# Kernel tuning notes

Hardware: AMD Instinct MI355X
Metric: run time of the kernel (lower is better)

The kernel has to match this reference:

```python
import jax, jax.numpy as jnp
import numpy as np

N = 100000
E = 1600000
D_IN = 128
D_HID = 128
D_OUT = 64


def setup_inputs() -> dict:
    key = jax.random.key(0)
    ks = jax.random.split(key, 9)
    x = jax.random.normal(ks[0], (N, D_IN), dtype=jnp.float32)
    edge_index = jax.random.randint(ks[1], (2, E), 0, N, dtype=jnp.int64)
    edge_weight = jax.random.uniform(ks[2], (E,), dtype=jnp.float32)
    s1 = 1.0 / np.sqrt(D_IN)
    s2 = 1.0 / np.sqrt(D_HID)
    W1 = jax.random.uniform(ks[3], (D_IN, D_HID), jnp.float32, -s1, s1)
    b1 = jnp.zeros((D_HID,), jnp.float32)
    W2 = jax.random.uniform(ks[4], (D_HID, D_HID), jnp.float32, -s2, s2)
    b2 = jnp.zeros((D_HID,), jnp.float32)
    Wfc = jax.random.uniform(ks[5], (D_HID, D_OUT), jnp.float32, -s2, s2)
    bfc = jax.random.uniform(ks[6], (D_OUT,), jnp.float32, -s2, s2)
    return {"x": x, "edge_index": edge_index, "edge_weight": edge_weight,
            "W1": W1, "b1": b1, "W2": W2, "b2": b2, "Wfc": Wfc, "bfc": bfc}


def _gcn_layer(h, row, col, w, n, W, b):
    # h' = D^{-1/2} (A + I) D^{-1/2} h W + b  (PyG GCNConv with edge weights)
    h = h @ W  # [n, d_out]
    deg = jax.ops.segment_sum(w, col, num_segments=n)  # weighted in-degree incl. self loops
    dinv = jnp.where(deg > 0, jax.lax.rsqrt(deg), 0.0)
    norm = dinv[row] * w * dinv[col]  # [E+n]
    out = jax.ops.segment_sum(norm[:, None] * h[row], col, num_segments=n)
    return out + b


def reference(x, edge_index, edge_weight, W1, b1, W2, b2, Wfc, bfc):
    n = x.shape[0]
    loop = jnp.arange(n, dtype=edge_index.dtype)
    row = jnp.concatenate([edge_index[0], loop])  # sources (+ self loops)
    col = jnp.concatenate([edge_index[1], loop])  # destinations
    w = jnp.concatenate([edge_weight, jnp.ones((n,), edge_weight.dtype)])
    h = jax.nn.relu(_gcn_layer(x, row, col, w, n, W1, b1))
    h = jax.nn.relu(_gcn_layer(h, row, col, w, n, W2, b2))
    return jax.nn.sigmoid(h @ Wfc + bfc)
```

## Files before the change

### kernel.cpp

```cpp
#include <hip/hip_runtime.h>
#include <math.h>

#define N_NODES 100000
#define N_EDGES 1600000
#define SCAN_CHUNK 1024
#define NSCAN ((N_NODES + SCAN_CHUNK - 1) / SCAN_CHUNK)
#define WMASK ((1ull << 40) - 1)
#define LDSW 136

typedef short bf16x8 __attribute__((ext_vector_type(8)));
typedef float f32x4 __attribute__((ext_vector_type(4)));

__device__ __forceinline__ float2 bf2f(unsigned int u) {
    float2 r;
    r.x = __uint_as_float(u << 16);
    r.y = __uint_as_float(u & 0xffff0000u);
    return r;
}
__device__ __forceinline__ unsigned int f2bf2(float a, float b) {
    unsigned int ua = __float_as_uint(a), ub = __float_as_uint(b);
    ua += 0x7fffu + ((ua >> 16) & 1u);
    ub += 0x7fffu + ((ub >> 16) & 1u);
    return (ua >> 16) | (ub & 0xffff0000u);
}
__device__ __forceinline__ unsigned short f2bf(float a) {
    unsigned int u = __float_as_uint(a);
    u += 0x7fffu + ((u >> 16) & 1u);
    return (unsigned short)(u >> 16);
}

__global__ void k_detect(const int* __restrict__ ei, int* __restrict__ flag, int host_hint) {
    __shared__ int s_cnt;
    if (threadIdx.x == 0) s_cnt = 0;
    __syncthreads();
    int local = 0;
    for (int e = threadIdx.x; e < 4096; e += blockDim.x)
        if (ei[2 * e + 1] != 0) local++;
    atomicAdd(&s_cnt, local);
    __syncthreads();
    if (threadIdx.x == 0) flag[0] = (host_hint || s_cnt < 100) ? 1 : 0;
}

__global__ void k_init(unsigned long long* __restrict__ packed) {
    int i = blockIdx.x * blockDim.x + threadIdx.x;
    if (i < N_NODES) packed[i] = 0ull;
}

__global__ void k_hist(const int* __restrict__ ei32, const int* __restrict__ flag,
                       const float* __restrict__ w,
                       unsigned long long* __restrict__ packed) {
    int e = blockIdx.x * blockDim.x + threadIdx.x;
    if (e >= N_EDGES) return;
    int c;
    if (flag[0]) {
        const long long* ei64 = (const long long*)ei32;
        c = (int)ei64[N_EDGES + e];
    } else {
        c = ei32[N_EDGES + e];
    }
    unsigned long long wfix = (unsigned long long)(w[e] * 4294967296.0f);
    atomicAdd(&packed[c], (1ull << 40) | wfix);
}

__global__ __launch_bounds__(256) void k_scan_a(const unsigned long long* __restrict__ packed,
                                                int* __restrict__ cnt,
                                                float* __restrict__ dinv,
                                                int* __restrict__ bsum) {
    __shared__ int sred[4];
    const int b = blockIdx.x, tid = threadIdx.x;
    const int base = b * SCAN_CHUNK;
    int s = 0;
    #pragma unroll
    for (int i = 0; i < 4; i++) {
        int idx = base + tid + i * 256;
        if (idx < N_NODES) {
            unsigned long long p = packed[idx];
            int c = (int)(p >> 40);
            float deg = 1.0f + (float)(p & WMASK) * 2.3283064365386963e-10f;
            cnt[idx] = c;
            dinv[idx] = rsqrtf(deg);
            s += c;
        }
    }
    #pragma unroll
    for (int sh = 1; sh < 64; sh <<= 1) s += __shfl_xor(s, sh);
    if ((tid & 63) == 0) sred[tid >> 6] = s;
    __syncthreads();
    if (tid == 0) bsum[b] = sred[0] + sred[1] + sred[2] + sred[3];
}

__global__ __launch_bounds__(128) void k_scan_b(const int* __restrict__ bsum,
                                                int* __restrict__ bex) {
    __shared__ int wsum[2];
    const int tid = threadIdx.x, lane = tid & 63, w = tid >> 6;
    int v = (tid < NSCAN) ? bsum[tid] : 0;
    int x = v;
    #pragma unroll
    for (int sh = 1; sh < 64; sh <<= 1) {
        int t = __shfl_up(x, sh);
        if (lane >= sh) x += t;
    }
    if (lane == 63) wsum[w] = x;
    __syncthreads();
    int add = (w == 1) ? wsum[0] : 0;
    if (tid < NSCAN) bex[tid] = x - v + add;
}

__global__ __launch_bounds__(256) void k_scan_c(const int* __restrict__ cnt,
                                                const int* __restrict__ bex,
                                                int* __restrict__ off,
                                                int* __restrict__ cur) {
    __shared__ int swave[4];
    const int b = blockIdx.x, tid = threadIdx.x;
    const int base = b * SCAN_CHUNK + tid * 4;
    int4 v = make_int4(0, 0, 0, 0);
    if (base + 3 < N_NODES) v = *(const int4*)&cnt[base];
    else {
        if (base + 0 < N_NODES) v.x = cnt[base + 0];
        if (base + 1 < N_NODES) v.y = cnt[base + 1];
        if (base + 2 < N_NODES) v.z = cnt[base + 2];
    }
    const int tsum = v.x + v.y + v.z + v.w;
    const int lane = tid & 63, w = tid >> 6;
    int x = tsum;
    #pragma unroll
    for (int sh = 1; sh < 64; sh <<= 1) {
        int t = __shfl_up(x, sh);
        if (lane >= sh) x += t;
    }
    if (lane == 63) swave[w] = x;
    __syncthreads();
    int wadd = 0;
    for (int i = 0; i < w; i++) wadd += swave[i];
    const int ex = bex[b] + wadd + (x - tsum);
    const int p0 = ex, p1 = p0 + v.x, p2 = p1 + v.y, p3 = p2 + v.z;
    if (base + 3 < N_NODES) {
        *(int4*)&off[base] = make_int4(p0, p1, p2, p3);
        *(int4*)&cur[base] = make_int4(p0, p1, p2, p3);
    } else {
        if (base + 0 < N_NODES) { off[base + 0] = p0; cur[base + 0] = p0; }
        if (base + 1 < N_NODES) { off[base + 1] = p1; cur[base + 1] = p1; }
        if (base + 2 < N_NODES) { off[base + 2] = p2; cur[base + 2] = p2; }
    }
}

__global__ void k_scatter(const int* __restrict__ ei32, const int* __restrict__ flag,
                          const float* __restrict__ w, const float* __restrict__ dinv,
                          int* __restrict__ cursor, unsigned int* __restrict__ sedge) {
    int e = blockIdx.x * blockDim.x + threadIdx.x;
    if (e >= N_EDGES) return;
    int r, c;
    if (flag[0]) {
        const long long* ei64 = (const long long*)ei32;
        r = (int)ei64[e];
        c = (int)ei64[N_EDGES + e];
    } else {
        r = ei32[e];
        c = ei32[N_EDGES + e];
    }
    float coef = dinv[r] * w[e] * dinv[c];
    unsigned int q = (unsigned int)(coef * 32767.0f + 0.5f);
    int p = atomicAdd(&cursor[c], 1);
    sedge[p] = ((unsigned int)r << 15) | q;
}

__global__ void k_castw(const float* __restrict__ W, unsigned short* __restrict__ Wt) {
    int i = blockIdx.x * blockDim.x + threadIdx.x;
    int k = i >> 7, n = i & 127;
    Wt[n * 128 + k] = f2bf(W[k * 128 + n]);
}

template <bool ABF16>
__global__ __launch_bounds__(256) void k_gemm_mfma(const void* __restrict__ Av,
                                                   const unsigned short* __restrict__ Wt,
                                                   unsigned short* __restrict__ Cb) {
    __shared__ unsigned short Al[128 * LDSW];
    __shared__ unsigned short Wl[128 * LDSW];
    const int tid = threadIdx.x;
    const int srow = tid >> 1, h = tid & 1;
    const int r0 = blockIdx.x * 128;

    {
        const uint4* src = (const uint4*)&Wt[srow * 128 + h * 64];
        uint4* dst = (uint4*)&Wl[srow * LDSW + h * 64];
        #pragma unroll
        for (int c = 0; c < 8; c++) dst[c] = src[c];
    }
    {
        const bool ok = (r0 + srow) < N_NODES;
        uint4* dst = (uint4*)&Al[srow * LDSW + h * 64];
        if constexpr (ABF16) {
            const uint4* src = (const uint4*)((const unsigned short*)Av +
                                              (size_t)(r0 + srow) * 128 + h * 64);
            uint4 z = make_uint4(0, 0, 0, 0);
            #pragma unroll
            for (int c = 0; c < 8; c++) dst[c] = ok ? src[c] : z;
        } else {
            const float* src = (const float*)Av + (size_t)(r0 + srow) * 128 + h * 64;
            #pragma unroll
            for (int c = 0; c < 8; c++) {
                float4 f0 = ok ? *(const float4*)&src[c * 8]     : make_float4(0, 0, 0, 0);
                float4 f1 = ok ? *(const float4*)&src[c * 8 + 4] : make_float4(0, 0, 0, 0);
                uint4 pk;
                pk.x = f2bf2(f0.x, f0.y);
                pk.y = f2bf2(f0.z, f0.w);
                pk.z = f2bf2(f1.x, f1.y);
                pk.w = f2bf2(f1.z, f1.w);
                dst[c] = pk;
            }
        }
    }
    __syncthreads();

    const int lane = tid & 63;
    const int w = tid >> 6;
    const int lr = lane & 15;
    const int kg = lane >> 4;
    f32x4 acc[2][8] = {};

    #pragma unroll
    for (int k0 = 0; k0 < 128; k0 += 32) {
        const int kb = k0 + kg * 8;
        bf16x8 a0 = *(const bf16x8*)&Al[(w * 32 + lr) * LDSW + kb];
        bf16x8 a1 = *(const bf16x8*)&Al[(w * 32 + 16 + lr) * LDSW + kb];
        #pragma unroll
        for (int ct = 0; ct < 8; ct++) {
            bf16x8 b = *(const bf16x8*)&Wl[(ct * 16 + lr) * LDSW + kb];
            acc[0][ct] = __builtin_amdgcn_mfma_f32_16x16x32_bf16(a0, b, acc[0][ct], 0, 0, 0);
            acc[1][ct] = __builtin_amdgcn_mfma_f32_16x16x32_bf16(a1, b, acc[1][ct], 0, 0, 0);
        }
    }

    #pragma unroll
    for (int rt = 0; rt < 2; rt++)
        #pragma unroll
        for (int r = 0; r < 4; r++) {
            int row = r0 + w * 32 + rt * 16 + kg * 4 + r;
            if (row < N_NODES) {
                #pragma unroll
                for (int ct = 0; ct < 8; ct++)
                    Cb[(size_t)row * 128 + ct * 16 + lr] = f2bf(acc[rt][ct][r]);
            }
        }
}

template <int DOUT>
__global__ __launch_bounds__(256) void k_gemm(const float* __restrict__ A,
                                              const float* __restrict__ W,
                                              const float* __restrict__ bias,
                                              float* __restrict__ C) {
    constexpr int CPT = DOUT / 16;
    __shared__ float Ws[128 * DOUT];
    __shared__ float As[8][128];
    const int tid = threadIdx.x;
    const int tx = tid & 15, ty = tid >> 4;

    for (int i = tid * 4; i < 128 * DOUT; i += 256 * 4)
        *(float4*)&Ws[i] = *(const float4*)&W[i];

    const int r0 = blockIdx.x * 128;
    const int arow = tid >> 1;
    const int ak = (tid & 1) * 4;
    const bool rowok = (r0 + arow) < N_NODES;

    float acc[8][CPT];
    #pragma unroll
    for (int i = 0; i < 8; i++)
        #pragma unroll
        for (int j = 0; j < CPT; j++) acc[i][j] = 0.f;

    for (int k0 = 0; k0 < 128; k0 += 8) {
        float4 av = make_float4(0.f, 0.f, 0.f, 0.f);
        if (rowok) av = *(const float4*)&A[(size_t)(r0 + arow) * 128 + k0 + ak];
        __syncthreads();
        As[ak + 0][arow] = av.x;
        As[ak + 1][arow] = av.y;
        As[ak + 2][arow] = av.z;
        As[ak + 3][arow] = av.w;
        __syncthreads();
        #pragma unroll
        for (int kk = 0; kk < 8; kk++) {
            float4 a0 = *(const float4*)&As[kk][ty * 8];
            float4 a1 = *(const float4*)&As[kk][ty * 8 + 4];
            float av8[8] = {a0.x, a0.y, a0.z, a0.w, a1.x, a1.y, a1.z, a1.w};
            float wv[CPT];
            float4 w0 = *(const float4*)&Ws[(k0 + kk) * DOUT + tx * CPT];
            wv[0] = w0.x; wv[1] = w0.y; wv[2] = w0.z; wv[3] = w0.w;
            #pragma unroll
            for (int i = 0; i < 8; i++)
                #pragma unroll
                for (int j = 0; j < CPT; j++)
                    acc[i][j] = fmaf(av8[i], wv[j], acc[i][j]);
        }
    }

    #pragma unroll
    for (int i = 0; i < 8; i++) {
        int r = r0 + ty * 8 + i;
        if (r < N_NODES) {
            float vout[CPT];
            #pragma unroll
            for (int j = 0; j < CPT; j++) {
                float v = acc[i][j] + bias[tx * CPT + j];
                vout[j] = 1.0f / (1.0f + expf(-v));
            }
            #pragma unroll
            for (int j = 0; j < CPT; j += 4)
                *(float4*)&C[(size_t)r * DOUT + tx * CPT + j] =
                    make_float4(vout[j], vout[j + 1], vout[j + 2], vout[j + 3]);
        }
    }
}

template <bool OBF16>
__global__ __launch_bounds__(256) void k_aggregate(const unsigned int* __restrict__ lin,
                                                   const unsigned int* __restrict__ sedge,
                                                   const int* __restrict__ off,
                                                   const int* __restrict__ cnt,
                                                   const float* __restrict__ dinv,
                                                   const float* __restrict__ bias,
                                                   void* __restrict__ outv) {
    const int node = (blockIdx.x * 256 + threadIdx.x) >> 6;
    const int lane = threadIdx.x & 63;
    if (node >= N_NODES) return;
    const float di = dinv[node];
    float2 sv = bf2f(lin[(size_t)node * 64 + lane]);
    float ax = di * di * sv.x;
    float ay = di * di * sv.y;
    const int start = __builtin_amdgcn_readfirstlane(off[node]);
    const int end = start + __builtin_amdgcn_readfirstlane(cnt[node]);
    for (int e0 = start; e0 < end; e0 += 8) {
        unsigned int en[8];
        #pragma unroll
        for (int i = 0; i < 8; i++) {
            int idx = e0 + i;
            en[i] = sedge[idx < end ? idx : end - 1];
        }
        float2 v[8];
        #pragma unroll
        for (int i = 0; i < 8; i++)
            v[i] = bf2f(lin[(size_t)(en[i] >> 15) * 64 + lane]);
        #pragma unroll
        for (int i = 0; i < 8; i++) {
            float cf = (e0 + i < end) ? (float)(en[i] & 0x7fffu) * 3.051850947599719e-05f : 0.0f;
            ax = fmaf(cf, v[i].x, ax);
            ay = fmaf(cf, v[i].y, ay);
        }
    }
    const int lane2 = lane * 2;
    float2 bv = *(const float2*)&bias[lane2];
    ax = fmaxf(ax + bv.x, 0.f);
    ay = fmaxf(ay + bv.y, 0.f);
    if constexpr (OBF16) {
        ((unsigned int*)outv)[(size_t)node * 64 + lane] = f2bf2(ax, ay);
    } else {
        *(float2*)&((float*)outv)[(size_t)node * 128 + lane2] = make_float2(ax, ay);
    }
}

extern "C" void kernel_launch(void* const* d_in, const int* in_sizes, int n_in,
                              void* d_out, int out_size, void* d_ws, size_t ws_size,
                              hipStream_t stream) {
    const float* x   = (const float*)d_in[0];
    const int*   ei  = (const int*)d_in[1];
    const float* ew  = (const float*)d_in[2];
    const float* W1  = (const float*)d_in[3];
    const float* b1  = (const float*)d_in[4];
    const float* W2  = (const float*)d_in[5];
    const float* b2  = (const float*)d_in[6];
    const float* Wfc = (const float*)d_in[7];
    const float* bfc = (const float*)d_in[8];
    float* out = (float*)d_out;

    char* ws = (char*)d_ws;
    size_t o = 0;
    auto alloc = [&](size_t bytes) { char* p = ws + o; o += (bytes + 255) & ~255ull; return p; };
    unsigned long long* packed = (unsigned long long*)alloc((size_t)N_NODES * 8);
    float* dinv  = (float*)alloc((size_t)N_NODES * 4);
    int*   cnt   = (int*)  alloc((size_t)N_NODES * 4);
    int*   off   = (int*)  alloc((size_t)N_NODES * 4);
    int*   cur   = (int*)  alloc((size_t)N_NODES * 4);
    int*   flag  = (int*)  alloc(256);
    int*   bsum  = (int*)  alloc((size_t)NSCAN * 4);
    int*   bex   = (int*)  alloc((size_t)NSCAN * 4);
    unsigned int*   sedge = (unsigned int*)alloc((size_t)N_EDGES * 4);
    unsigned short* W1t   = (unsigned short*)alloc(128 * 128 * 2);
    unsigned short* W2t   = (unsigned short*)alloc(128 * 128 * 2);
    unsigned short* hbf   = (unsigned short*)alloc((size_t)N_NODES * 128 * 2);
    unsigned short* aggb  = (unsigned short*)alloc((size_t)N_NODES * 128 * 2);
    float*          aggf  = (float*)alloc((size_t)N_NODES * 128 * 4);

    const int EB = (N_EDGES + 255) / 256;
    const int NB = (N_NODES + 255) / 256;

    int hint64 = (in_sizes[1] == 4 * N_EDGES) ? 1 : 0;
    k_detect<<<1, 256, 0, stream>>>(ei, flag, hint64);
    k_init<<<NB, 256, 0, stream>>>(packed);
    k_castw<<<64, 256, 0, stream>>>(W1, W1t);
    k_castw<<<64, 256, 0, stream>>>(W2, W2t);
    k_hist<<<EB, 256, 0, stream>>>(ei, flag, ew, packed);
    k_scan_a<<<NSCAN, 256, 0, stream>>>(packed, cnt, dinv, bsum);
    k_scan_b<<<1, 128, 0, stream>>>(bsum, bex);
    k_scan_c<<<NSCAN, 256, 0, stream>>>(cnt, bex, off, cur);
    k_scatter<<<EB, 256, 0, stream>>>(ei, flag, ew, dinv, cur, sedge);

    const int GB = (N_NODES + 127) / 128;
    const int AB = (N_NODES * 64 + 255) / 256;

    k_gemm_mfma<false><<<GB, 256, 0, stream>>>(x, W1t, hbf);
    k_aggregate<true><<<AB, 256, 0, stream>>>((const unsigned int*)hbf, sedge, off, cnt, dinv, b1, aggb);
    k_gemm_mfma<true><<<GB, 256, 0, stream>>>(aggb, W2t, hbf);
    k_aggregate<false><<<AB, 256, 0, stream>>>((const unsigned int*)hbf, sedge, off, cnt, dinv, b2, aggf);
    k_gemm<64><<<GB, 256, 0, stream>>>(aggf, Wfc, bfc, out);
}
```

Before: 480.7 us.

## Bin edges by destination range before CSR scatter to localize writes

```diff
diff --git a/kernel.cpp b/kernel.cpp
--- a/kernel.cpp
+++ b/kernel.cpp
@@ -7,6 +7,11 @@
 #define NSCAN ((N_NODES + SCAN_CHUNK - 1) / SCAN_CHUNK)
 #define WMASK ((1ull << 40) - 1)
 #define LDSW 136
+#define BINSHIFT 9
+#define NBINS 196
+#define BINCAP 12288
+#define BIN_BLOCKS 512
+#define EPT 13
 
 typedef short bf16x8 __attribute__((ext_vector_type(8)));
 typedef float f32x4 __attribute__((ext_vector_type(4)));
@@ -41,25 +46,65 @@
     if (threadIdx.x == 0) flag[0] = (host_hint || s_cnt < 100) ? 1 : 0;
 }
 
-__global__ void k_init(unsigned long long* __restrict__ packed) {
+__global__ void k_init(unsigned long long* __restrict__ packed, int* __restrict__ gbincur) {
     int i = blockIdx.x * blockDim.x + threadIdx.x;
     if (i < N_NODES) packed[i] = 0ull;
-}
-
-__global__ void k_hist(const int* __restrict__ ei32, const int* __restrict__ flag,
-                       const float* __restrict__ w,
-                       unsigned long long* __restrict__ packed) {
-    int e = blockIdx.x * blockDim.x + threadIdx.x;
-    if (e >= N_EDGES) return;
-    int c;
-    if (flag[0]) {
-        const long long* ei64 = (const long long*)ei32;
-        c = (int)ei64[N_EDGES + e];
-    } else {
-        c = ei32[N_EDGES + e];
-    }
-    unsigned long long wfix = (unsigned long long)(w[e] * 4294967296.0f);
-    atomicAdd(&packed[c], (1ull << 40) | wfix);
+    if (i < NBINS) gbincur[i] = i * BINCAP;
+}
+
+__global__ __launch_bounds__(256) void k_bin(const int* __restrict__ ei32,
+                                             const int* __restrict__ flag,
+                                             const float* __restrict__ ew,
+                                             unsigned long long* __restrict__ packed,
+                                             int* __restrict__ gbincur,
+                                             uint2* __restrict__ binstage) {
+    __shared__ int scnt[256];
+    __shared__ int sbase[256];
+    const int tid = threadIdx.x;
+    scnt[tid] = 0;
+    const bool f64 = flag[0] != 0;
+    const long long base = (long long)blockIdx.x * (256 * EPT);
+    unsigned int ea[EPT], eb[EPT];
+    __syncthreads();
+    #pragma unroll
+    for (int i = 0; i < EPT; i++) {
+        long long e = base + (long long)i * 256 + tid;
+        bool ok = e < N_EDGES;
+        int r = 0, c = 0;
+        float w = 0.f;
+        if (ok) {
+            if (f64) {
+                const long long* p64 = (const long long*)ei32;
+                r = (int)p64[e];
+                c = (int)p64[N_EDGES + e];
+            } else {
+                r = ei32[e];
+                c = ei32[N_EDGES + e];
+            }
+            w = ew[e];
+            unsigned long long wfix = (unsigned long long)(w * 4294967296.0f);
+            atomicAdd(&packed[c], (1ull << 40) | wfix);
+            atomicAdd(&scnt[c >> BINSHIFT], 1);
+        }
+        unsigned int wq = (unsigned int)(w * 32767.0f + 0.5f);
+        ea[i] = ok ? (((unsigned int)c << 15) | wq) : 0xffffffffu;
+        eb[i] = (unsigned int)r;
+    }
+    __syncthreads();
+    {
+        int n = scnt[tid];
+        if (tid < NBINS && n > 0) sbase[tid] = atomicAdd(&gbincur[tid], n);
+        scnt[tid] = 0;
+    }
+    __syncthreads();
+    #pragma unroll
+    for (int i = 0; i < EPT; i++) {
+        if (ea[i] != 0xffffffffu) {
+            int bin = (int)(ea[i] >> (15 + BINSHIFT));
+            int slot = atomicAdd(&scnt[bin], 1);
+            binstage[sbase[bin] + slot] = make_uint2(ea[i], eb[i]);
+        }
+    }
 }
 
 __global__ __launch_bounds__(256) void k_scan_a(const unsigned long long* __restrict__ packed,
@@ -144,24 +189,26 @@
     }
 }
 
-__global__ void k_scatter(const int* __restrict__ ei32, const int* __restrict__ flag,
-                          const float* __restrict__ w, const float* __restrict__ dinv,
-                          int* __restrict__ cursor, unsigned int* __restrict__ sedge) {
-    int e = blockIdx.x * blockDim.x + threadIdx.x;
-    if (e >= N_EDGES) return;
-    int r, c;
-    if (flag[0]) {
-        const long long* ei64 = (const long long*)ei32;
-        r = (int)ei64[e];
-        c = (int)ei64[N_EDGES + e];
-    } else {
-        r = ei32[e];
-        c = ei32[N_EDGES + e];
-    }
-    float coef = dinv[r] * w[e] * dinv[c];
-    unsigned int q = (unsigned int)(coef * 32767.0f + 0.5f);
-    int p = atomicAdd(&cursor[c], 1);
-    sedge[p] = ((unsigned int)r << 15) | q;
+__global__ __launch_bounds__(256) void k_csr(const int* __restrict__ gbincur,
+                                             const uint2* __restrict__ binstage,
+                                             const float* __restrict__ dinv,
+                                             int* __restrict__ cur,
+                                             unsigned int* __restrict__ sedge) {
+    const int bin = blockIdx.x >> 1;
+    const int half = blockIdx.x & 1;
+    const int s0 = bin * BINCAP;
+    const int total = gbincur[bin] - s0;
+    for (int i = half * 256 + threadIdx.x; i < total; i += 512) {
+        uint2 en = binstage[s0 + i];
+        int c = (int)(en.x >> 15);
+        float w = (float)(en.x & 0x7fffu) * 3.051850947599719e-05f;
+        int r = (int)en.y;
+        float coef = dinv[c] * dinv[r] * w;
+        unsigned int q = (unsigned int)(coef * 32767.0f + 0.5f);
+        if (q > 32767u) q = 32767u;
+        int p = atomicAdd(&cur[c], 1);
+        sedge[p] = ((unsigned int)r << 15) | q;
+    }
 }
 
 __global__ void k_castw(const float* __restrict__ W, unsigned short* __restrict__ Wt) {
@@ -383,26 +430,28 @@
     int*   flag  = (int*)  alloc(256);
     int*   bsum  = (int*)  alloc((size_t)NSCAN * 4);
     int*   bex   = (int*)  alloc((size_t)NSCAN * 4);
+    int*   gbincur = (int*)alloc(256 * 4);
     unsigned int*   sedge = (unsigned int*)alloc((size_t)N_EDGES * 4);
     unsigned short* W1t   = (unsigned short*)alloc(128 * 128 * 2);
     unsigned short* W2t   = (unsigned short*)alloc(128 * 128 * 2);
-    unsigned short* hbf   = (unsigned short*)alloc((size_t)N_NODES * 128 * 2);
-    unsigned short* aggb  = (unsigned short*)alloc((size_t)N_NODES * 128 * 2);
-    float*          aggf  = (float*)alloc((size_t)N_NODES * 128 * 4);
-
-    const int EB = (N_EDGES + 255) / 256;
+    char* region1 = alloc((size_t)N_NODES * 128 * 2);
+    uint2*          binstage = (uint2*)region1;
+    unsigned short* hbf      = (unsigned short*)region1;
+    float*          aggf = (float*)alloc((size_t)N_NODES * 128 * 4);
+    unsigned short* aggb = (unsigned short*)aggf;
+
     const int NB = (N_NODES + 255) / 256;
 
     int hint64 = (in_sizes[1] == 4 * N_EDGES) ? 1 : 0;
     k_detect<<<1, 256, 0, stream>>>(ei, flag, hint64);
-    k_init<<<NB, 256, 0, stream>>>(packed);
+    k_init<<<NB, 256, 0, stream>>>(packed, gbincur);
     k_castw<<<64, 256, 0, stream>>>(W1, W1t);
     k_castw<<<64, 256, 0, stream>>>(W2, W2t);
-    k_hist<<<EB, 256, 0, stream>>>(ei, flag, ew, packed);
+    k_bin<<<BIN_BLOCKS, 256, 0, stream>>>(ei, flag, ew, packed, gbincur, binstage);
     k_scan_a<<<NSCAN, 256, 0, stream>>>(packed, cnt, dinv, bsum);
     k_scan_b<<<1, 128, 0, stream>>>(bsum, bex);
     k_scan_c<<<NSCAN, 256, 0, stream>>>(cnt, bex, off, cur);
-    k_scatter<<<EB, 256, 0, stream>>>(ei, flag, ew, dinv, cur, sedge);
+    k_csr<<<NBINS * 2, 256, 0, stream>>>(gbincur, binstage, dinv, cur, sedge);
 
     const int GB = (N_NODES + 127) / 128;
     const int AB = (N_NODES * 64 + 255) / 256;
```

Measured after the change: 452.6 us. 5.8% less time.
